# Optimization experiments

Hardware: AMD Instinct MI355X
Metric: run time of the kernel (lower is better)

## Reference

```python
import jax, jax.numpy as jnp
import numpy as np


def fake_quant(w, bits):
    # Symmetric per-tensor fake quantization with straight-through estimator.
    qmax = 2.0 ** (bits - 1) - 1.0
    scale = jnp.max(jnp.abs(w)) / qmax
    wq = jnp.clip(jnp.round(w / scale), -qmax, qmax) * scale
    return w + jax.lax.stop_gradient(wq - w)


def setup_inputs() -> dict:
    key = jax.random.key(0)
    k = jax.random.split(key, 5)
    B, S, D, H = 64, 196, 768, 3072
    x = jax.random.normal(k[0], (B, S, D), dtype=jnp.float32)
    w1 = jax.random.normal(k[1], (H, D), dtype=jnp.float32) * (1.0 / np.sqrt(D))
    b1 = jax.random.normal(k[2], (H,), dtype=jnp.float32) * 0.01
    w2 = jax.random.normal(k[3], (D, H), dtype=jnp.float32) * (1.0 / np.sqrt(H))
    b2 = jax.random.normal(k[4], (D,), dtype=jnp.float32) * 0.01
    return {"x": x, "w1": w1, "b1": b1, "w2": w2, "b2": b2, "bits": 8}


def reference(x, w1, b1, w2, b2, bits):
    # fc1 (fake-quant weight) -> ReLU -> fc2 (fake-quant weight)
    w1q = fake_quant(w1, bits)
    w2q = fake_quant(w2, bits)
    h = jnp.einsum('bsd,hd->bsh', x, w1q) + b1   # [B,S,3072]
    h = jax.nn.relu(h)
    out = jnp.einsum('bsh,dh->bsd', h, w2q) + b2  # [B,S,768]
    return out
```

## Files before the change

### kernel.cpp

```cpp
#include <hip/hip_runtime.h>
#include <hip/hip_bf16.h>
#include <stdint.h>

typedef __attribute__((ext_vector_type(8))) short bf16x8;
typedef __attribute__((ext_vector_type(4))) float f32x4;

__device__ __forceinline__ unsigned short f2bf(float f) {
  __hip_bfloat16 h = __float2bfloat16(f);
  return *reinterpret_cast<unsigned short*>(&h);
}

__global__ void absmax2_kernel(const float* __restrict__ w1, const float* __restrict__ w2,
                               int n4, unsigned int* __restrict__ out) {
  const float* w = blockIdx.y ? w2 : w1;
  __shared__ unsigned int red[256];
  unsigned int m = 0u;
  const uint4* w4 = reinterpret_cast<const uint4*>(w);
  for (int i = blockIdx.x * blockDim.x + threadIdx.x; i < n4;
       i += gridDim.x * blockDim.x) {
    uint4 v = w4[i];
    m = max(m, v.x & 0x7fffffffu);
    m = max(m, v.y & 0x7fffffffu);
    m = max(m, v.z & 0x7fffffffu);
    m = max(m, v.w & 0x7fffffffu);
  }
  red[threadIdx.x] = m;
  __syncthreads();
  for (int s = 128; s > 0; s >>= 1) {
    if ((int)threadIdx.x < s)
      red[threadIdx.x] = max(red[threadIdx.x], red[threadIdx.x + s]);
    __syncthreads();
  }
  if (threadIdx.x == 0) atomicMax(out + blockIdx.y, red[0]);
}

__global__ void quantcast_kernel(const float* __restrict__ w1, const float* __restrict__ w2,
                                 const float* __restrict__ x,
                                 int n4w, int n4x,
                                 const unsigned int* __restrict__ maxbits,
                                 const int* __restrict__ bits,
                                 unsigned short* __restrict__ o1,
                                 unsigned short* __restrict__ o2,
                                 unsigned short* __restrict__ ox) {
  if (blockIdx.y == 2) {
    const float4* x4 = reinterpret_cast<const float4*>(x);
    ushort4* o4 = reinterpret_cast<ushort4*>(ox);
    for (int i = blockIdx.x * blockDim.x + threadIdx.x; i < n4x;
         i += gridDim.x * blockDim.x) {
      float4 v = x4[i];
      o4[i] = make_ushort4(f2bf(v.x), f2bf(v.y), f2bf(v.z), f2bf(v.w));
    }
    return;
  }
  const float* w = blockIdx.y ? w2 : w1;
  unsigned short* o = blockIdx.y ? o2 : o1;
  const float qmax = (float)((1 << (*bits - 1)) - 1);
  const float scale = __uint_as_float(maxbits[blockIdx.y]) / qmax;
  const float4* w4 = reinterpret_cast<const float4*>(w);
  ushort4* o4 = reinterpret_cast<ushort4*>(o);
  for (int i = blockIdx.x * blockDim.x + threadIdx.x; i < n4w;
       i += gridDim.x * blockDim.x) {
    float4 v = w4[i];
    float a = fminf(fmaxf(rintf(v.x / scale), -qmax), qmax) * scale;
    float b = fminf(fmaxf(rintf(v.y / scale), -qmax), qmax) * scale;
    float c = fminf(fmaxf(rintf(v.z / scale), -qmax), qmax) * scale;
    float d = fminf(fmaxf(rintf(v.w / scale), -qmax), qmax) * scale;
    o4[i] = make_ushort4(f2bf(a), f2bf(b), f2bf(c), f2bf(d));
  }
}

template<bool RELU, bool BF16_OUT>
__global__ __launch_bounds__(256, 2)
void gemm_bt(const unsigned short* __restrict__ A,
             const unsigned short* __restrict__ B,
             const float* __restrict__ bias,
             void* __restrict__ Cout,
             int M, int N, int K, int gx) {
  constexpr int BM = 256, BN = 128, BK = 32;
  __shared__ __attribute__((aligned(16))) unsigned short As[2][BM * BK];
  __shared__ __attribute__((aligned(16))) unsigned short Bs[2][BN * BK];

  const int nwg = gridDim.x;
  const int orig = blockIdx.x;
  const int q = nwg >> 3, r = nwg & 7;
  const int xcd = orig & 7, cidx = orig >> 3;
  const int wgid = (xcd < r ? xcd * (q + 1) : r * (q + 1) + (xcd - r) * q) + cidx;
  const int bx = wgid % gx;
  const int by = wgid / gx;

  const int tid = threadIdx.x;
  const int lane = tid & 63;
  const int wave = tid >> 6;
  const int wr = wave >> 1;
  const int wc = wave & 1;
  const long brow = (long)by * BM;
  const long bcol = (long)bx * BN;

  f32x4 acc[8][4] = {};

  const int srow = lane >> 2;
  const int gslot = ((lane & 3) ^ ((lane >> 3) & 3)) * 8;
  const int fr = lane & 15;
  const int fs = lane >> 4;

  auto stage = [&](int k0, int b) {
#pragma unroll
    for (int it = 0; it < 4; ++it) {
      const int c = it * 4 + wave;
      const unsigned short* ga = A + (brow + c * 16 + srow) * (long)K + k0 + gslot;
      __builtin_amdgcn_global_load_lds(
          (const __attribute__((address_space(1))) void*)ga,
          (__attribute__((address_space(3))) void*)(&As[b][c * 512]), 16, 0, 0);
    }
#pragma unroll
    for (int it = 0; it < 2; ++it) {
      const int c = it * 4 + wave;
      const unsigned short* gb = B + (bcol + c * 16 + srow) * (long)K + k0 + gslot;
      __builtin_amdgcn_global_load_lds(
          (const __attribute__((address_space(1))) void*)gb,
          (__attribute__((address_space(3))) void*)(&Bs[b][c * 512]), 16, 0, 0);
    }
  };

  const int nt = K / BK;
  stage(0, 0);
  stage(BK, 1);

  for (int t = 0; t < nt; ++t) {
    const int b = t & 1;
    if (t < nt - 1) asm volatile("s_waitcnt vmcnt(6)" ::: "memory");
    else            asm volatile("s_waitcnt vmcnt(0)" ::: "memory");
    __builtin_amdgcn_s_barrier();

    const unsigned short* as = &As[b][0];
    const unsigned short* bs = &Bs[b][0];
    bf16x8 a[8], bb[4];
#pragma unroll
    for (int m = 0; m < 8; ++m) {
      const int row = wr * 128 + m * 16 + fr;
      a[m] = *reinterpret_cast<const bf16x8*>(as + row * BK + ((fs ^ ((row >> 1) & 3)) * 8));
    }
#pragma unroll
    for (int n = 0; n < 4; ++n) {
      const int row = wc * 64 + n * 16 + fr;
      bb[n] = *reinterpret_cast<const bf16x8*>(bs + row * BK + ((fs ^ ((row >> 1) & 3)) * 8));
    }
#pragma unroll
    for (int m = 0; m < 8; ++m)
#pragma unroll
      for (int n = 0; n < 4; ++n)
        acc[m][n] = __builtin_amdgcn_mfma_f32_16x16x32_bf16(a[m], bb[n], acc[m][n], 0, 0, 0);

    asm volatile("s_waitcnt lgkmcnt(0)" ::: "memory");
    __builtin_amdgcn_sched_barrier(0);
    __builtin_amdgcn_s_barrier();
    if (t + 2 < nt) stage((t + 2) * BK, b);
  }

  const int fq = lane >> 4;
#pragma unroll
  for (int n = 0; n < 4; ++n) {
    const long col = bcol + wc * 64 + n * 16 + fr;
    const float bv = bias[col];
#pragma unroll
    for (int m = 0; m < 8; ++m) {
#pragma unroll
      for (int rr = 0; rr < 4; ++rr) {
        const long row = brow + wr * 128 + m * 16 + fq * 4 + rr;
        float v = acc[m][n][rr] + bv;
        if (RELU) v = fmaxf(v, 0.0f);
        if (BF16_OUT)
          ((unsigned short*)Cout)[row * N + col] = f2bf(v);
        else
          ((float*)Cout)[row * N + col] = v;
      }
    }
  }
}

extern "C" void kernel_launch(void* const* d_in, const int* in_sizes, int n_in,
                              void* d_out, int out_size, void* d_ws, size_t ws_size,
                              hipStream_t stream) {
  const float* x  = (const float*)d_in[0];
  const float* w1 = (const float*)d_in[1];
  const float* b1 = (const float*)d_in[2];
  const float* w2 = (const float*)d_in[3];
  const float* b2 = (const float*)d_in[4];
  const int* bits = (const int*)d_in[5];

  const int M = 64 * 196;
  const int D = 768, H = 3072;
  const int nx = M * D;
  const int nw1 = H * D;
  const int nw2 = D * H;

  char* ws = (char*)d_ws;
  unsigned int* scales = (unsigned int*)ws;
  unsigned short* xb  = (unsigned short*)(ws + 256);
  unsigned short* w1q = (unsigned short*)(ws + 256 + (size_t)nx * 2);
  unsigned short* w2q = (unsigned short*)(ws + 256 + (size_t)nx * 2 + (size_t)nw1 * 2);
  unsigned short* hb  = (unsigned short*)(ws + 256 + (size_t)nx * 2 + (size_t)(nw1 + nw2) * 2);

  hipMemsetAsync(scales, 0, 8, stream);
  absmax2_kernel<<<dim3(512, 2), 256, 0, stream>>>(w1, w2, nw1 / 4, scales);
  quantcast_kernel<<<dim3(768, 3), 256, 0, stream>>>(w1, w2, x, nw1 / 4, nx / 4,
                                                     scales, bits, w1q, w2q, xb);

  gemm_bt<true, true><<<(M / 256) * (H / 128), 256, 0, stream>>>(
      xb, w1q, b1, hb, M, H, D, H / 128);
  gemm_bt<false, false><<<(M / 256) * (D / 128), 256, 0, stream>>>(
      hb, w2q, b2, d_out, M, D, H, D / 128);
}
```

Before: 222.9 us.

## Switch GEMMs to 256x256 tiles with 8 waves and interleaved K-half pipelining

```diff
diff --git a/kernel.cpp b/kernel.cpp
--- a/kernel.cpp
+++ b/kernel.cpp
@@ -70,15 +70,13 @@
 }
 
 template<bool RELU, bool BF16_OUT>
-__global__ __launch_bounds__(256, 2)
-void gemm_bt(const unsigned short* __restrict__ A,
-             const unsigned short* __restrict__ B,
-             const float* __restrict__ bias,
-             void* __restrict__ Cout,
-             int M, int N, int K, int gx) {
-  constexpr int BM = 256, BN = 128, BK = 32;
-  __shared__ __attribute__((aligned(16))) unsigned short As[2][BM * BK];
-  __shared__ __attribute__((aligned(16))) unsigned short Bs[2][BN * BK];
+__global__ __launch_bounds__(512, 2)
+void gemm8w(const unsigned short* __restrict__ A,
+            const unsigned short* __restrict__ B,
+            const float* __restrict__ bias,
+            void* __restrict__ Cout,
+            int M, int N, int K, int gx) {
+  extern __shared__ unsigned short lds[];
 
   const int nwg = gridDim.x;
   const int orig = blockIdx.x;
@@ -91,83 +89,122 @@
   const int tid = threadIdx.x;
   const int lane = tid & 63;
   const int wave = tid >> 6;
-  const int wr = wave >> 1;
-  const int wc = wave & 1;
-  const long brow = (long)by * BM;
-  const long bcol = (long)bx * BN;
+  const int wr = wave >> 2;
+  const int wc = wave & 3;
+  const long brow = (long)by * 256;
+  const long bcol = (long)bx * 256;
 
   f32x4 acc[8][4] = {};
 
-  const int srow = lane >> 2;
-  const int gslot = ((lane & 3) ^ ((lane >> 3) & 3)) * 8;
   const int fr = lane & 15;
-  const int fs = lane >> 4;
-
-  auto stage = [&](int k0, int b) {
-#pragma unroll
-    for (int it = 0; it < 4; ++it) {
-      const int c = it * 4 + wave;
-      const unsigned short* ga = A + (brow + c * 16 + srow) * (long)K + k0 + gslot;
+  const int fq = lane >> 4;
+  const int swz8 = ((lane & 3) ^ ((lane >> 3) & 3)) * 8;
+  const int sgrow = wave * 16 + (lane >> 2);
+
+  auto SA = [&](int t, int kh) {
+    unsigned short* dst = lds + ((t & 1) * 2 + kh) * 8192 + wave * 16 * 32;
+    const unsigned short* g = A + (brow + sgrow) * (long)K + t * 64 + kh * 32 + swz8;
+#pragma unroll
+    for (int c = 0; c < 2; ++c)
       __builtin_amdgcn_global_load_lds(
-          (const __attribute__((address_space(1))) void*)ga,
-          (__attribute__((address_space(3))) void*)(&As[b][c * 512]), 16, 0, 0);
-    }
-#pragma unroll
-    for (int it = 0; it < 2; ++it) {
-      const int c = it * 4 + wave;
-      const unsigned short* gb = B + (bcol + c * 16 + srow) * (long)K + k0 + gslot;
+          (const __attribute__((address_space(1))) void*)(g + (long)c * 128 * K),
+          (__attribute__((address_space(3))) void*)(dst + c * 128 * 32), 16, 0, 0);
+  };
+  auto SB = [&](int t, int kh) {
+    unsigned short* dst = lds + 32768 + ((t & 1) * 2 + kh) * 8192 + wave * 16 * 32;
+    const unsigned short* g = B + (bcol + sgrow) * (long)K + t * 64 + kh * 32 + swz8;
+#pragma unroll
+    for (int c = 0; c < 2; ++c)
       __builtin_amdgcn_global_load_lds(
-          (const __attribute__((address_space(1))) void*)gb,
-          (__attribute__((address_space(3))) void*)(&Bs[b][c * 512]), 16, 0, 0);
-    }
-  };
-
-  const int nt = K / BK;
-  stage(0, 0);
-  stage(BK, 1);
-
+          (const __attribute__((address_space(1))) void*)(g + (long)c * 128 * K),
+          (__attribute__((address_space(3))) void*)(dst + c * 128 * 32), 16, 0, 0);
+  };
+
+  auto RDA = [&](int b, int ks, int mseg, bf16x8* a) {
+    const unsigned short* base = lds + (b * 2 + ks) * 8192;
+#pragma unroll
+    for (int mi = 0; mi < 4; ++mi) {
+      const int row = wr * 128 + mseg * 64 + mi * 16 + fr;
+      a[mi] = *reinterpret_cast<const bf16x8*>(base + row * 32 + ((fq ^ ((row >> 1) & 3)) * 8));
+    }
+  };
+  auto RDB = [&](int b, int ks, bf16x8* bb) {
+    const unsigned short* base = lds + 32768 + (b * 2 + ks) * 8192;
+#pragma unroll
+    for (int ni = 0; ni < 4; ++ni) {
+      const int row = wc * 64 + ni * 16 + fr;
+      bb[ni] = *reinterpret_cast<const bf16x8*>(base + row * 32 + ((fq ^ ((row >> 1) & 3)) * 8));
+    }
+  };
+  auto MM = [&](int mseg, bf16x8* a, bf16x8* bb) {
+#pragma unroll
+    for (int mi = 0; mi < 4; ++mi)
+#pragma unroll
+      for (int ni = 0; ni < 4; ++ni)
+        acc[mseg * 4 + mi][ni] = __builtin_amdgcn_mfma_f32_16x16x32_bf16(
+            a[mi], bb[ni], acc[mseg * 4 + mi][ni], 0, 0, 0);
+  };
+
+  const int nt = K / 64;
+  SA(0, 0); SB(0, 0); SA(0, 1); SB(0, 1); SA(1, 0); SB(1, 0);
+
+  bf16x8 a[4], bb[4];
   for (int t = 0; t < nt; ++t) {
     const int b = t & 1;
-    if (t < nt - 1) asm volatile("s_waitcnt vmcnt(6)" ::: "memory");
-    else            asm volatile("s_waitcnt vmcnt(0)" ::: "memory");
-    __builtin_amdgcn_s_barrier();
-
-    const unsigned short* as = &As[b][0];
-    const unsigned short* bs = &Bs[b][0];
-    bf16x8 a[8], bb[4];
-#pragma unroll
-    for (int m = 0; m < 8; ++m) {
-      const int row = wr * 128 + m * 16 + fr;
-      a[m] = *reinterpret_cast<const bf16x8*>(as + row * BK + ((fs ^ ((row >> 1) & 3)) * 8));
-    }
-#pragma unroll
-    for (int n = 0; n < 4; ++n) {
-      const int row = wc * 64 + n * 16 + fr;
-      bb[n] = *reinterpret_cast<const bf16x8*>(bs + row * BK + ((fs ^ ((row >> 1) & 3)) * 8));
-    }
-#pragma unroll
-    for (int m = 0; m < 8; ++m)
-#pragma unroll
-      for (int n = 0; n < 4; ++n)
-        acc[m][n] = __builtin_amdgcn_mfma_f32_16x16x32_bf16(a[m], bb[n], acc[m][n], 0, 0, 0);
-
-    asm volatile("s_waitcnt lgkmcnt(0)" ::: "memory");
-    __builtin_amdgcn_sched_barrier(0);
-    __builtin_amdgcn_s_barrier();
-    if (t + 2 < nt) stage((t + 2) * BK, b);
-  }
-
-  const int fq = lane >> 4;
-#pragma unroll
-  for (int n = 0; n < 4; ++n) {
-    const long col = bcol + wc * 64 + n * 16 + fr;
+    if (t + 1 < nt) {
+      SA(t + 1, 1);
+      asm volatile("s_waitcnt vmcnt(10)" ::: "memory");
+    } else {
+      asm volatile("s_waitcnt vmcnt(4)" ::: "memory");
+    }
+    asm volatile("s_barrier" ::: "memory");
+    RDA(b, 0, 0, a); RDB(b, 0, bb);
+    asm volatile("s_waitcnt lgkmcnt(0)" ::: "memory");
+    __builtin_amdgcn_sched_barrier(0);
+    __builtin_amdgcn_s_setprio(1);
+    MM(0, a, bb);
+    __builtin_amdgcn_s_setprio(0);
+    asm volatile("s_barrier" ::: "memory");
+    if (t + 1 < nt) SB(t + 1, 1);
+    RDA(b, 0, 1, a);
+    asm volatile("s_waitcnt lgkmcnt(0)" ::: "memory");
+    __builtin_amdgcn_sched_barrier(0);
+    __builtin_amdgcn_s_setprio(1);
+    MM(1, a, bb);
+    __builtin_amdgcn_s_setprio(0);
+    asm volatile("s_barrier" ::: "memory");
+    if (t + 2 < nt) SA(t + 2, 0);
+    if (t + 3 <= nt)      asm volatile("s_waitcnt vmcnt(10)" ::: "memory");
+    else if (t == nt - 2) asm volatile("s_waitcnt vmcnt(8)"  ::: "memory");
+    else                  asm volatile("s_waitcnt vmcnt(0)"  ::: "memory");
+    asm volatile("s_barrier" ::: "memory");
+    RDA(b, 1, 0, a); RDB(b, 1, bb);
+    asm volatile("s_waitcnt lgkmcnt(0)" ::: "memory");
+    __builtin_amdgcn_sched_barrier(0);
+    __builtin_amdgcn_s_setprio(1);
+    MM(0, a, bb);
+    __builtin_amdgcn_s_setprio(0);
+    asm volatile("s_barrier" ::: "memory");
+    if (t + 2 < nt) SB(t + 2, 0);
+    RDA(b, 1, 1, a);
+    asm volatile("s_waitcnt lgkmcnt(0)" ::: "memory");
+    __builtin_amdgcn_sched_barrier(0);
+    __builtin_amdgcn_s_setprio(1);
+    MM(1, a, bb);
+    __builtin_amdgcn_s_setprio(0);
+    asm volatile("s_barrier" ::: "memory");
+  }
+
+#pragma unroll
+  for (int ni = 0; ni < 4; ++ni) {
+    const long col = bcol + wc * 64 + ni * 16 + fr;
     const float bv = bias[col];
 #pragma unroll
-    for (int m = 0; m < 8; ++m) {
+    for (int mi = 0; mi < 8; ++mi) {
 #pragma unroll
       for (int rr = 0; rr < 4; ++rr) {
-        const long row = brow + wr * 128 + m * 16 + fq * 4 + rr;
-        float v = acc[m][n][rr] + bv;
+        const long row = brow + wr * 128 + mi * 16 + fq * 4 + rr;
+        float v = acc[mi][ni][rr] + bv;
         if (RELU) v = fmaxf(v, 0.0f);
         if (BF16_OUT)
           ((unsigned short*)Cout)[row * N + col] = f2bf(v);
@@ -192,22 +229,30 @@
   const int D = 768, H = 3072;
   const int nx = M * D;
   const int nw1 = H * D;
-  const int nw2 = D * H;
 
   char* ws = (char*)d_ws;
   unsigned int* scales = (unsigned int*)ws;
   unsigned short* xb  = (unsigned short*)(ws + 256);
   unsigned short* w1q = (unsigned short*)(ws + 256 + (size_t)nx * 2);
   unsigned short* w2q = (unsigned short*)(ws + 256 + (size_t)nx * 2 + (size_t)nw1 * 2);
-  unsigned short* hb  = (unsigned short*)(ws + 256 + (size_t)nx * 2 + (size_t)(nw1 + nw2) * 2);
+  unsigned short* hb  = (unsigned short*)(ws + 256 + (size_t)nx * 2 + (size_t)nw1 * 4);
+
+  static bool attr_done = false;
+  if (!attr_done) {
+    hipFuncSetAttribute((const void*)gemm8w<true, true>,
+                        hipFuncAttributeMaxDynamicSharedMemorySize, 131072);
+    hipFuncSetAttribute((const void*)gemm8w<false, false>,
+                        hipFuncAttributeMaxDynamicSharedMemorySize, 131072);
+    attr_done = true;
+  }
 
   hipMemsetAsync(scales, 0, 8, stream);
   absmax2_kernel<<<dim3(512, 2), 256, 0, stream>>>(w1, w2, nw1 / 4, scales);
   quantcast_kernel<<<dim3(768, 3), 256, 0, stream>>>(w1, w2, x, nw1 / 4, nx / 4,
                                                      scales, bits, w1q, w2q, xb);
 
-  gemm_bt<true, true><<<(M / 256) * (H / 128), 256, 0, stream>>>(
-      xb, w1q, b1, hb, M, H, D, H / 128);
-  gemm_bt<false, false><<<(M / 256) * (D / 128), 256, 0, stream>>>(
-      hb, w2q, b2, d_out, M, D, H, D / 128);
-}
+  gemm8w<true, true><<<(M / 256) * (H / 256), 512, 131072, stream>>>(
+      xb, w1q, b1, hb, M, H, D, H / 256);
+  gemm8w<false, false><<<(M / 256) * (D / 256), 512, 131072, stream>>>(
+      hb, w2q, b2, d_out, M, D, H, D / 256);
+}
```

Result: faster. 208.5 us (-6.5%).
